# Kernel tuning notes

Measured on AMD Instinct MI355X. Metric: run time of the kernel, lower is better.

## Reference

```python
import jax, jax.numpy as jnp
import numpy as np

C = 64        # in_channels
E = 64        # embed_dim
K_RATIO = 0.5


def _conv(x, w, b, pad, groups):
    # x: [B,C,H,W], w: [O, I/groups, kh, kw] (torch OIHW layout)
    y = jax.lax.conv_general_dilated(
        x, w, window_strides=(1, 1), padding=[(pad, pad), (pad, pad)],
        dimension_numbers=("NCHW", "OIHW", "NCHW"), feature_group_count=groups)
    return y + b[None, :, None, None]


def setup_inputs() -> dict:
    key = jax.random.key(0)
    ks = jax.random.split(key, 16)
    s = 0.05
    return {
        "x": jax.random.normal(ks[0], (8, C, 64, 64), jnp.float32),
        "w1": jax.random.normal(ks[1], (C, C, 1, 1), jnp.float32) * s,
        "b1": jax.random.normal(ks[2], (C,), jnp.float32) * s,
        "w3": jax.random.normal(ks[3], (C, 1, 3, 3), jnp.float32) * s,
        "b3": jax.random.normal(ks[4], (C,), jnp.float32) * s,
        "w5": jax.random.normal(ks[5], (C, 1, 5, 5), jnp.float32) * s,
        "b5": jax.random.normal(ks[6], (C,), jnp.float32) * s,
        "qw": jax.random.normal(ks[7], (E, 3 * C), jnp.float32) * s,
        "qb": jax.random.normal(ks[8], (E,), jnp.float32) * s,
        "kw": jax.random.normal(ks[9], (E, 3 * C), jnp.float32) * s,
        "kb": jax.random.normal(ks[10], (E,), jnp.float32) * s,
        "vw": jax.random.normal(ks[11], (C, 3 * C), jnp.float32) * s,
        "vb": jax.random.normal(ks[12], (C,), jnp.float32) * s,
        "ow": jax.random.normal(ks[13], (C, C), jnp.float32) * s,
        "ob": jax.random.normal(ks[14], (C,), jnp.float32) * s,
    }


def reference(x, w1, b1, w3, b3, w5, b5, qw, qb, kw, kb, vw, vb, ow, ob):
    b, c, h, w = x.shape
    N = h * w
    f1 = _conv(x, w1, b1, pad=0, groups=1)        # 1x1 conv
    f2 = _conv(x, w3, b3, pad=1, groups=c)        # 3x3 depthwise
    f3 = _conv(x, w5, b5, pad=2, groups=c)        # 5x5 depthwise
    f_multi = jnp.concatenate([f1, f2, f3], axis=1)           # [b, 3c, h, w]
    f_flat = f_multi.reshape(b, 3 * c, N).transpose(0, 2, 1)  # [b, N, 3c]

    Q = jnp.einsum("bnd,ed->bne", f_flat, qw) + qb            # [b, N, E]
    K = jnp.einsum("bnd,ed->bne", f_flat, kw) + kb            # [b, N, E]
    V = jnp.einsum("bnd,cd->bnc", f_flat, vw) + vb            # [b, N, c]

    attn = jnp.einsum("bqe,bke->bqk", Q, K) / jnp.sqrt(jnp.float32(E))
    attn = jax.nn.softmax(attn, axis=-1)                      # [b, N, N]

    key_importance = attn.sum(axis=1)                         # [b, N]
    k_val = max(1, min(int(N * K_RATIO), N))
    _, topk_idx = jax.lax.top_k(key_importance, k_val)        # [b, k_val]
    mask = jnp.zeros_like(key_importance).at[
        jnp.arange(b)[:, None], topk_idx].set(1.0)            # [b, N]

    attn_c = attn * mask[:, None, :]
    attn_c = attn_c / (attn_c.sum(axis=-1, keepdims=True) + 1e-8)
    out = jnp.einsum("bqk,bkc->bqc", attn_c, V)               # [b, N, c]
    out = jnp.einsum("bnc,oc->bno", out, ow) + ob
    return out.transpose(0, 2, 1).reshape(b, c, h, w)
```

## Files before the change

### kernel.cpp

```cpp
#include <hip/hip_runtime.h>
#include <hip/hip_bf16.h>

typedef unsigned short ushort;
typedef __bf16 bf16x8 __attribute__((ext_vector_type(8)));
typedef float f32x4 __attribute__((ext_vector_type(4)));

__device__ __forceinline__ ushort f2bu(float f) {
  __hip_bfloat16 h = __float2bfloat16(f);
  return *(ushort*)&h;
}
__device__ __forceinline__ f32x4 mfma16(bf16x8 a, bf16x8 b, f32x4 c) {
  return __builtin_amdgcn_mfma_f32_16x16x32_bf16(a, b, c, 0, 0, 0);
}
__device__ __forceinline__ float fexp2(float x) { return __builtin_amdgcn_exp2f(x); }


__global__ __launch_bounds__(256) void k_conv(
    const float* __restrict__ x, const float* __restrict__ w1, const float* __restrict__ b1,
    const float* __restrict__ w3, const float* __restrict__ b3,
    const float* __restrict__ w5, const float* __restrict__ b5,
    ushort* __restrict__ f) {
  __shared__ float xs[64][64];
  __shared__ float w1s[64 * 65];
  __shared__ float w3s[576];
  __shared__ float w5s[1600];
  __shared__ float bs1[64], bs3[64], bs5[64];
  const int tid = threadIdx.x;
  const int y = blockIdx.x;
  const int b = blockIdx.y;
  for (int i = tid; i < 4096; i += 256) {
    int ch = i >> 6, w = i & 63;
    xs[ch][w] = x[((size_t)(b * 64 + ch) * 64 + y) * 64 + w];
  }
  for (int i = tid; i < 4096; i += 256) w1s[(i >> 6) * 65 + (i & 63)] = w1[i];
  for (int i = tid; i < 576; i += 256) w3s[i] = w3[i];
  for (int i = tid; i < 1600; i += 256) w5s[i] = w5[i];
  if (tid < 64) { bs1[tid] = b1[tid]; bs3[tid] = b3[tid]; bs5[tid] = b5[tid]; }
  __syncthreads();
  const int px = tid & 63;
  const int cg = tid >> 6;
  const int cb = cg * 16;
  ushort* fo = f + ((size_t)b * 4096 + y * 64 + px) * 192;
  float a1[16];
#pragma unroll
  for (int j = 0; j < 16; j++) a1[j] = bs1[cb + j];
  for (int ic = 0; ic < 64; ic++) {
    float xv = xs[ic][px];
#pragma unroll
    for (int j = 0; j < 16; j++) a1[j] += w1s[(cb + j) * 65 + ic] * xv;
  }
#pragma unroll
  for (int j = 0; j < 16; j++) fo[cb + j] = f2bu(a1[j]);
#pragma unroll 4
  for (int j = 0; j < 16; j++) {
    int c = cb + j;
    const float* xc = x + (size_t)(b * 64 + c) * 4096;
    float a3 = bs3[c], a5 = bs5[c];
#pragma unroll
    for (int dy = 0; dy < 5; dy++) {
      int yy = y + dy - 2;
      if (yy < 0 || yy >= 64) continue;
      const float* xr = xc + yy * 64;
#pragma unroll
      for (int dx = 0; dx < 5; dx++) {
        int wx = px + dx - 2;
        float v = (wx >= 0 && wx < 64) ? xr[wx] : 0.f;
        a5 += w5s[c * 25 + dy * 5 + dx] * v;
        if (dy >= 1 && dy <= 3 && dx >= 1 && dx <= 3)
          a3 += w3s[c * 9 + (dy - 1) * 3 + (dx - 1)] * v;
      }
    }
    fo[64 + c] = f2bu(a3);
    fo[128 + c] = f2bu(a5);
  }
}

__global__ __launch_bounds__(256) void k_w2b(
    const float* __restrict__ qw, const float* __restrict__ kw,
    const float* __restrict__ vw, ushort* __restrict__ Wb) {
  int i = blockIdx.x * 256 + threadIdx.x;
  const float* src = (i < 12288) ? qw : (i < 24576) ? kw : vw;
  int off = (i < 12288) ? i : (i < 24576) ? (i - 12288) : (i - 24576);
  Wb[i] = f2bu(src[off]);
}

__global__ __launch_bounds__(256) void k_qkv(
    const ushort* __restrict__ F, const ushort* __restrict__ Wb,
    const float* __restrict__ qb, const float* __restrict__ kb,
    const float* __restrict__ vb,
    ushort* __restrict__ Q, ushort* __restrict__ K, ushort* __restrict__ V) {
  __shared__ __align__(16) ushort fs[64][200];
  const int tid = threadIdx.x;
  const int w = tid >> 6;
  const int lane = tid & 63;
  const int col = lane & 15;
  const int quad = lane >> 4;
  const size_t rowbase = (size_t)blockIdx.x * 64;
  for (int i = tid; i < 1536; i += 256) {
    int r = i / 24, c8 = i % 24;
    *(uint4*)&fs[r][c8 * 8] = *(const uint4*)&F[rowbase * 192 + (size_t)i * 8];
  }
  __syncthreads();
  bf16x8 af[6];
#pragma unroll
  for (int kk = 0; kk < 6; kk++)
    af[kk] = *(const bf16x8*)&fs[w * 16 + col][kk * 32 + quad * 8];
  ushort* const outp[3] = {Q, K, V};
  const float* const bp[3] = {qb, kb, vb};
#pragma unroll
  for (int sel = 0; sel < 3; sel++) {
    const ushort* wsel = Wb + sel * 12288;
    const float sc = (sel == 0) ? 0.125f * 1.44269504088896f : 1.0f;
#pragma unroll
    for (int ntl = 0; ntl < 4; ntl++) {
      const ushort* brow = wsel + (ntl * 16 + col) * 192 + quad * 8;
      f32x4 acc = {0.f, 0.f, 0.f, 0.f};
#pragma unroll
      for (int kk = 0; kk < 6; kk++) {
        bf16x8 bf = *(const bf16x8*)&brow[kk * 32];
        acc = mfma16(af[kk], bf, acc);
      }
      float bv = bp[sel][ntl * 16 + col];
#pragma unroll
      for (int r = 0; r < 4; r++)
        outp[sel][(rowbase + w * 16 + quad * 4 + r) * 64 + ntl * 16 + col] =
            f2bu((acc[r] + bv) * sc);
    }
  }
}

__global__ __launch_bounds__(256) void k_sumexp_l(
    const ushort* __restrict__ Qb, const ushort* __restrict__ Kb,
    float* __restrict__ Lp) {
  __shared__ float red[4][64];
  const int tid = threadIdx.x;
  const int b = blockIdx.x & 7;
  const int rest = blockIdx.x >> 3;
  const int qt = rest & 63;
  const int kh = rest >> 6;
  const int lane = tid & 63;
  const int w = tid >> 6;
  const int col = lane & 15;
  const int quad = lane >> 4;
  const size_t qbase = (size_t)b * 4096 + qt * 64;
  const size_t kbase = (size_t)b * 4096 + kh * 2048;
  bf16x8 af[4][2];
#pragma unroll
  for (int t = 0; t < 4; t++)
#pragma unroll
    for (int h = 0; h < 2; h++)
      af[t][h] = *(const bf16x8*)&Qb[(qbase + t * 16 + col) * 64 + quad * 8 + h * 32];
  const ushort* kp = &Kb[(kbase + w * 16 + col) * 64 + quad * 8];
  float lacc[4][4];
#pragma unroll
  for (int t = 0; t < 4; t++)
#pragma unroll
    for (int r = 0; r < 4; r++) lacc[t][r] = 0.f;
  bf16x8 nb0 = *(const bf16x8*)kp;
  bf16x8 nb1 = *(const bf16x8*)(kp + 32);
#pragma unroll 1
  for (int kt = 0; kt < 32; kt++) {
    bf16x8 b0 = nb0, b1 = nb1;
    if (kt < 31) {
      nb0 = *(const bf16x8*)(kp + (size_t)(kt + 1) * 4096);
      nb1 = *(const bf16x8*)(kp + (size_t)(kt + 1) * 4096 + 32);
    }
#pragma unroll
    for (int t = 0; t < 4; t++) {
      f32x4 acc = {0.f, 0.f, 0.f, 0.f};
      acc = mfma16(af[t][0], b0, acc);
      acc = mfma16(af[t][1], b1, acc);
#pragma unroll
      for (int r = 0; r < 4; r++) lacc[t][r] += fexp2(acc[r]);
    }
  }
#pragma unroll
  for (int t = 0; t < 4; t++)
#pragma unroll
    for (int r = 0; r < 4; r++) {
      float v = lacc[t][r];
      v += __shfl_xor(v, 1); v += __shfl_xor(v, 2);
      v += __shfl_xor(v, 4); v += __shfl_xor(v, 8);
      if (col == 0) red[w][t * 16 + quad * 4 + r] = v;
    }
  __syncthreads();
  if (tid < 64) {
    float l = red[0][tid] + red[1][tid] + red[2][tid] + red[3][tid];
    Lp[((size_t)(b * 64 + qt) * 2 + kh) * 64 + tid] = l;
  }
}

__global__ __launch_bounds__(256) void k_lcomb(
    const float* __restrict__ Lp, float* __restrict__ Lo, float* __restrict__ Linv) {
  int i = blockIdx.x * 256 + threadIdx.x;
  int bqt = i >> 6, q = i & 63;
  float l = Lp[(size_t)bqt * 128 + q] + Lp[(size_t)bqt * 128 + 64 + q];
  Lo[i] = l;
  Linv[i] = 1.f / l;
}

__global__ __launch_bounds__(256) void k_sumexp_ip(
    const ushort* __restrict__ Qb, const ushort* __restrict__ Kb,
    const float* __restrict__ Linv, float* __restrict__ IP) {
  __shared__ float lred[64];
  const int tid = threadIdx.x;
  const int b = blockIdx.x & 7;
  const int rest = blockIdx.x >> 3;
  const int qt = rest & 63;
  const int kh = rest >> 6;
  const int lane = tid & 63;
  const int w = tid >> 6;
  const int col = lane & 15;
  const int quad = lane >> 4;
  const size_t qbase = (size_t)b * 4096 + qt * 64;
  const size_t kbase = (size_t)b * 4096 + kh * 2048;
  if (tid < 64) lred[tid] = Linv[qbase + tid];
  bf16x8 af[4][2];
#pragma unroll
  for (int t = 0; t < 4; t++)
#pragma unroll
    for (int h = 0; h < 2; h++)
      af[t][h] = *(const bf16x8*)&Qb[(qbase + t * 16 + col) * 64 + quad * 8 + h * 32];
  __syncthreads();
  float linv[4][4];
#pragma unroll
  for (int t = 0; t < 4; t++)
#pragma unroll
    for (int r = 0; r < 4; r++) linv[t][r] = lred[t * 16 + quad * 4 + r];
  const ushort* kp = &Kb[(kbase + w * 16 + col) * 64 + quad * 8];
  bf16x8 nb0 = *(const bf16x8*)kp;
  bf16x8 nb1 = *(const bf16x8*)(kp + 32);
#pragma unroll 1
  for (int kt = 0; kt < 32; kt++) {
    bf16x8 b0 = nb0, b1 = nb1;
    if (kt < 31) {
      nb0 = *(const bf16x8*)(kp + (size_t)(kt + 1) * 4096);
      nb1 = *(const bf16x8*)(kp + (size_t)(kt + 1) * 4096 + 32);
    }
    float ip = 0.f;
#pragma unroll
    for (int t = 0; t < 4; t++) {
      f32x4 acc = {0.f, 0.f, 0.f, 0.f};
      acc = mfma16(af[t][0], b0, acc);
      acc = mfma16(af[t][1], b1, acc);
#pragma unroll
      for (int r = 0; r < 4; r++) ip += fexp2(acc[r]) * linv[t][r];
    }
    ip += __shfl_xor(ip, 16);
    ip += __shfl_xor(ip, 32);
    if (quad == 0)
      IP[((size_t)(b * 64 + qt)) * 4096 + (kh * 32 + kt) * 64 + w * 16 + col] = ip;
  }
}

__global__ __launch_bounds__(256) void k_impsum(
    const float* __restrict__ IP, float* __restrict__ imp) {
  const int tid = threadIdx.x;
  const int b = blockIdx.y;
  const int col = blockIdx.x * 256 + tid;
  const float* p = IP + (size_t)b * 64 * 4096 + col;
  float s = 0.f;
#pragma unroll 8
  for (int r = 0; r < 64; r++) s += p[(size_t)r * 4096];
  imp[(size_t)b * 4096 + col] = s;
}

__global__ __launch_bounds__(256) void k_mask2c(
    const float* __restrict__ imp, const ushort* __restrict__ Kb,
    const ushort* __restrict__ Vb, ushort* __restrict__ Kc,
    ushort* __restrict__ Vc) {
  __shared__ __align__(16) float imps[4096];
  __shared__ int part[4][64];
  const int tid = threadIdx.x;
  const int b = blockIdx.y;
  const int base = blockIdx.x * 64;
  for (int i = tid; i < 4096; i += 256) imps[i] = imp[(size_t)b * 4096 + i];
  __syncthreads();
  const int cand = tid & 63;
  const int seg = tid >> 6;
  const int k = base + cand;
  const float v = imps[k];
  int cnt = 0;
  const int j0 = seg * 1024;
  for (int j = j0; j < j0 + 1024; j += 4) {
    float4 a = *(const float4*)&imps[j];
    cnt += (a.x > v) ? 1 : ((a.x == v && (j + 0) < k) ? 1 : 0);
    cnt += (a.y > v) ? 1 : ((a.y == v && (j + 1) < k) ? 1 : 0);
    cnt += (a.z > v) ? 1 : ((a.z == v && (j + 2) < k) ? 1 : 0);
    cnt += (a.w > v) ? 1 : ((a.w == v && (j + 3) < k) ? 1 : 0);
  }
  part[seg][cand] = cnt;
  __syncthreads();
  const int c = part[0][cand] + part[1][cand] + part[2][cand] + part[3][cand];
  if (c < 2048) {
    const ushort* ksrc = &Kb[((size_t)b * 4096 + k) * 64 + seg * 16];
    const ushort* vsrc = &Vb[((size_t)b * 4096 + k) * 64 + seg * 16];
    ushort* kdst = &Kc[((size_t)b * 2048 + c) * 64 + seg * 16];
    ushort* vdst = &Vc[((size_t)b * 2048 + c) * 64 + seg * 16];
    *(uint4*)kdst = *(const uint4*)ksrc;
    *(uint4*)(kdst + 8) = *(const uint4*)(ksrc + 8);
    *(uint4*)vdst = *(const uint4*)vsrc;
    *(uint4*)(vdst + 8) = *(const uint4*)(vsrc + 8);
  }
}

__global__ __launch_bounds__(256) void k_attn_out(
    const ushort* __restrict__ Qb, const ushort* __restrict__ Kc,
    const ushort* __restrict__ Vc, const float* __restrict__ Lo,
    const float* __restrict__ owp, const float* __restrict__ obp,
    float* __restrict__ out) {
  __shared__ __align__(16) ushort Vt[64][72];
  __shared__ __align__(16) ushort Ps[64][72];
  __shared__ __align__(16) ushort ows[64][72];
  __shared__ float dred[4][64];
  __shared__ float lqs[64];
  const int tid = threadIdx.x;
  const int b = blockIdx.x & 7;
  const int qt = blockIdx.x >> 3;
  const int lane = tid & 63;
  const int w = tid >> 6;
  const int col = lane & 15;
  const int quad = lane >> 4;
  const size_t qbase = (size_t)b * 4096 + qt * 64;
  const size_t kbase = (size_t)b * 2048;
  bf16x8 af[4][2];
#pragma unroll
  for (int t = 0; t < 4; t++)
#pragma unroll
    for (int h = 0; h < 2; h++)
      af[t][h] = *(const bf16x8*)&Qb[(qbase + t * 16 + col) * 64 + quad * 8 + h * 32];
  for (int i = tid; i < 4096; i += 256) ows[i >> 6][i & 63] = f2bu(owp[i]);
  if (tid < 64) lqs[tid] = Lo[qbase + tid];
  f32x4 pv[4];
  float dpacc[4][4];
#pragma unroll
  for (int t = 0; t < 4; t++) {
    pv[t] = (f32x4){0.f, 0.f, 0.f, 0.f};
#pragma unroll
    for (int r = 0; r < 4; r++) dpacc[t][r] = 0.f;
  }
  const int vrow = tid & 63;
  const int vch = tid >> 6;
  const ushort* kp = &Kc[(kbase + w * 16 + col) * 64 + quad * 8];
  bf16x8 nb0 = *(const bf16x8*)kp;
  bf16x8 nb1 = *(const bf16x8*)(kp + 32);
  for (int kt = 0; kt < 32; kt++) {
    __syncthreads();
    {
      const ushort* vsrc = &Vc[(kbase + kt * 64 + vrow) * 64 + vch * 16];
      uint4 v0 = *(const uint4*)vsrc;
      uint4 v1 = *(const uint4*)(vsrc + 8);
      ushort tmp[16];
      *(uint4*)&tmp[0] = v0;
      *(uint4*)&tmp[8] = v1;
#pragma unroll
      for (int j = 0; j < 16; j++) Vt[vch * 16 + j][vrow] = tmp[j];
    }
    bf16x8 b0 = nb0, b1 = nb1;
    if (kt < 31) {
      nb0 = *(const bf16x8*)(kp + (size_t)(kt + 1) * 4096);
      nb1 = *(const bf16x8*)(kp + (size_t)(kt + 1) * 4096 + 32);
    }
#pragma unroll
    for (int t = 0; t < 4; t++) {
      f32x4 acc = {0.f, 0.f, 0.f, 0.f};
      acc = mfma16(af[t][0], b0, acc);
      acc = mfma16(af[t][1], b1, acc);
#pragma unroll
      for (int r = 0; r < 4; r++) {
        float p = fexp2(acc[r]);
        dpacc[t][r] += p;
        Ps[t * 16 + quad * 4 + r][w * 16 + col] = f2bu(p);
      }
    }
    __syncthreads();
    bf16x8 v0f = *(const bf16x8*)&Vt[w * 16 + col][quad * 8];
    bf16x8 v1f = *(const bf16x8*)&Vt[w * 16 + col][quad * 8 + 32];
#pragma unroll
    for (int t = 0; t < 4; t++) {
      bf16x8 p0 = *(const bf16x8*)&Ps[t * 16 + col][quad * 8];
      bf16x8 p1 = *(const bf16x8*)&Ps[t * 16 + col][quad * 8 + 32];
      pv[t] = mfma16(p0, v0f, pv[t]);
      pv[t] = mfma16(p1, v1f, pv[t]);
    }
  }
#pragma unroll
  for (int t = 0; t < 4; t++)
#pragma unroll
    for (int r = 0; r < 4; r++) {
      float v = dpacc[t][r];
      v += __shfl_xor(v, 1); v += __shfl_xor(v, 2);
      v += __shfl_xor(v, 4); v += __shfl_xor(v, 8);
      if (col == 0) dred[w][t * 16 + quad * 4 + r] = v;
    }
  __syncthreads();
#pragma unroll
  for (int t = 0; t < 4; t++)
#pragma unroll
    for (int r = 0; r < 4; r++) {
      int q = t * 16 + quad * 4 + r;
      float den = dred[0][q] + dred[1][q] + dred[2][q] + dred[3][q] + 1e-8f * lqs[q];
      Ps[q][w * 16 + col] = f2bu(pv[t][r] / den);
    }
  __syncthreads();
  bf16x8 w0 = *(const bf16x8*)&ows[w * 16 + col][quad * 8];
  bf16x8 w1 = *(const bf16x8*)&ows[w * 16 + col][quad * 8 + 32];
  const float obv = obp[w * 16 + col];
#pragma unroll
  for (int t = 0; t < 4; t++) {
    bf16x8 p0 = *(const bf16x8*)&Ps[t * 16 + col][quad * 8];
    bf16x8 p1 = *(const bf16x8*)&Ps[t * 16 + col][quad * 8 + 32];
    f32x4 oc = {0.f, 0.f, 0.f, 0.f};
    oc = mfma16(p0, w0, oc);
    oc = mfma16(p1, w1, oc);
#pragma unroll
    for (int r = 0; r < 4; r++) {
      int q = t * 16 + quad * 4 + r;
      int co = w * 16 + col;
      out[((size_t)(b * 64 + co)) * 4096 + qt * 64 + q] = oc[r] + obv;
    }
  }
}

extern "C" void kernel_launch(void* const* d_in, const int* in_sizes, int n_in,
                              void* d_out, int out_size, void* d_ws, size_t ws_size,
                              hipStream_t stream) {
  const float* x  = (const float*)d_in[0];
  const float* w1 = (const float*)d_in[1];
  const float* b1 = (const float*)d_in[2];
  const float* w3 = (const float*)d_in[3];
  const float* b3 = (const float*)d_in[4];
  const float* w5 = (const float*)d_in[5];
  const float* b5 = (const float*)d_in[6];
  const float* qw = (const float*)d_in[7];
  const float* qb = (const float*)d_in[8];
  const float* kw = (const float*)d_in[9];
  const float* kb = (const float*)d_in[10];
  const float* vw = (const float*)d_in[11];
  const float* vb = (const float*)d_in[12];
  const float* ow = (const float*)d_in[13];
  const float* ob = (const float*)d_in[14];
  float* out = (float*)d_out;
  float* ws = (float*)d_ws;
  ushort* F    = (ushort*)ws;
  ushort* Qb   = (ushort*)(ws + 3145728);
  ushort* Kb   = (ushort*)(ws + 4194304);
  ushort* Vb   = (ushort*)(ws + 5242880);
  float*  Lo   = ws + 6291456;
  float*  Linv = ws + 6324224;
  float*  Lp   = ws + 6356992;
  float*  IP   = ws + 6422528;
  float*  imp  = ws + 8519680;
  ushort* Kc   = (ushort*)(ws + 8552448);
  ushort* Vc   = (ushort*)(ws + 9076736);
  ushort* Wb   = (ushort*)(ws + 9601024);

  k_w2b<<<144, 256, 0, stream>>>(qw, kw, vw, Wb);
  k_conv<<<dim3(64, 8), 256, 0, stream>>>(x, w1, b1, w3, b3, w5, b5, F);
  k_qkv<<<512, 256, 0, stream>>>(F, Wb, qb, kb, vb, Qb, Kb, Vb);
  k_sumexp_l<<<1024, 256, 0, stream>>>(Qb, Kb, Lp);
  k_lcomb<<<128, 256, 0, stream>>>(Lp, Lo, Linv);
  k_sumexp_ip<<<1024, 256, 0, stream>>>(Qb, Kb, Linv, IP);
  k_impsum<<<dim3(16, 8), 256, 0, stream>>>(IP, imp);
  k_mask2c<<<dim3(64, 8), 256, 0, stream>>>(imp, Kb, Vb, Kc, Vc);
  k_attn_out<<<512, 256, 0, stream>>>(Qb, Kc, Vc, Lo, ow, ob, out);
}
```

Before: 333.8 us.

## Stage padded bf16 input rows in LDS for conv; read transposed 1x1 weights directly

The conv kernel now loads a 5-row halo of the input, converted to bf16, into shared memory with zero padding. The depthwise 3x3/5x5 taps read from LDS instead of strided global memory with bounds checks. The 1x1 conv weights are pre-transposed by the weight-conversion kernel and read with a wave-uniform index from global memory, which drops the weight and bias LDS staging. Rounding the input to bf16 before the convolutions adds precision loss, and each block reloads five rows, so input traffic goes up while the per-tap boundary branches disappear.

```diff
diff --git a/kernel.cpp b/kernel.cpp
--- a/kernel.cpp
+++ b/kernel.cpp
@@ -9,6 +9,10 @@
   __hip_bfloat16 h = __float2bfloat16(f);
   return *(ushort*)&h;
 }
+__device__ __forceinline__ float bu2f(ushort u) {
+  unsigned int v = ((unsigned int)u) << 16;
+  return __uint_as_float(v);
+}
 __device__ __forceinline__ f32x4 mfma16(bf16x8 a, bf16x8 b, f32x4 c) {
   return __builtin_amdgcn_mfma_f32_16x16x32_bf16(a, b, c, 0, 0, 0);
 }
@@ -16,58 +20,61 @@
 
 
 __global__ __launch_bounds__(256) void k_conv(
-    const float* __restrict__ x, const float* __restrict__ w1, const float* __restrict__ b1,
+    const float* __restrict__ x, const float* __restrict__ w1t, const float* __restrict__ b1,
     const float* __restrict__ w3, const float* __restrict__ b3,
     const float* __restrict__ w5, const float* __restrict__ b5,
     ushort* __restrict__ f) {
-  __shared__ float xs[64][64];
-  __shared__ float w1s[64 * 65];
-  __shared__ float w3s[576];
-  __shared__ float w5s[1600];
-  __shared__ float bs1[64], bs3[64], bs5[64];
+  __shared__ ushort Xs[5 * 64 * 74];
   const int tid = threadIdx.x;
   const int y = blockIdx.x;
   const int b = blockIdx.y;
-  for (int i = tid; i < 4096; i += 256) {
-    int ch = i >> 6, w = i & 63;
-    xs[ch][w] = x[((size_t)(b * 64 + ch) * 64 + y) * 64 + w];
-  }
-  for (int i = tid; i < 4096; i += 256) w1s[(i >> 6) * 65 + (i & 63)] = w1[i];
-  for (int i = tid; i < 576; i += 256) w3s[i] = w3[i];
-  for (int i = tid; i < 1600; i += 256) w5s[i] = w5[i];
-  if (tid < 64) { bs1[tid] = b1[tid]; bs3[tid] = b3[tid]; bs5[tid] = b5[tid]; }
+  for (int i = tid; i < 320 * 5; i += 256) {
+    int r = i / 5, pp = i % 5;
+    int col = (pp < 2) ? 2 * pp : 68 + 2 * (pp - 2);
+    *(unsigned int*)&Xs[r * 74 + col] = 0u;
+  }
+#pragma unroll
+  for (int k = 0; k < 20; k++) {
+    int idx = tid + k * 256;
+    int px4 = idx & 15, ch = (idx >> 4) & 63, yy = idx >> 10;
+    int ysrc = y + yy - 2;
+    float4 v = make_float4(0.f, 0.f, 0.f, 0.f);
+    if (ysrc >= 0 && ysrc < 64)
+      v = *(const float4*)&x[(((size_t)(b * 64 + ch) * 64) + ysrc) * 64 + px4 * 4];
+    unsigned int lo = (unsigned int)f2bu(v.x) | ((unsigned int)f2bu(v.y) << 16);
+    unsigned int hi = (unsigned int)f2bu(v.z) | ((unsigned int)f2bu(v.w) << 16);
+    int base = (yy * 64 + ch) * 74 + 4 + px4 * 4;
+    *(unsigned int*)&Xs[base] = lo;
+    *(unsigned int*)&Xs[base + 2] = hi;
+  }
   __syncthreads();
   const int px = tid & 63;
-  const int cg = tid >> 6;
-  const int cb = cg * 16;
+  const int cbu = __builtin_amdgcn_readfirstlane((tid >> 6) * 16);
   ushort* fo = f + ((size_t)b * 4096 + y * 64 + px) * 192;
   float a1[16];
 #pragma unroll
-  for (int j = 0; j < 16; j++) a1[j] = bs1[cb + j];
+  for (int j = 0; j < 16; j++) a1[j] = b1[cbu + j];
   for (int ic = 0; ic < 64; ic++) {
-    float xv = xs[ic][px];
-#pragma unroll
-    for (int j = 0; j < 16; j++) a1[j] += w1s[(cb + j) * 65 + ic] * xv;
-  }
-#pragma unroll
-  for (int j = 0; j < 16; j++) fo[cb + j] = f2bu(a1[j]);
+    float xv = bu2f(Xs[(2 * 64 + ic) * 74 + 4 + px]);
+    const float* wrow = &w1t[ic * 64 + cbu];
+#pragma unroll
+    for (int j = 0; j < 16; j++) a1[j] += wrow[j] * xv;
+  }
+#pragma unroll
+  for (int j = 0; j < 16; j++) fo[cbu + j] = f2bu(a1[j]);
 #pragma unroll 4
   for (int j = 0; j < 16; j++) {
-    int c = cb + j;
-    const float* xc = x + (size_t)(b * 64 + c) * 4096;
-    float a3 = bs3[c], a5 = bs5[c];
+    int c = cbu + j;
+    float a3 = b3[c], a5 = b5[c];
 #pragma unroll
     for (int dy = 0; dy < 5; dy++) {
-      int yy = y + dy - 2;
-      if (yy < 0 || yy >= 64) continue;
-      const float* xr = xc + yy * 64;
+      const ushort* row = &Xs[(dy * 64 + c) * 74 + 2 + px];
 #pragma unroll
       for (int dx = 0; dx < 5; dx++) {
-        int wx = px + dx - 2;
-        float v = (wx >= 0 && wx < 64) ? xr[wx] : 0.f;
-        a5 += w5s[c * 25 + dy * 5 + dx] * v;
+        float v = bu2f(row[dx]);
+        a5 += w5[c * 25 + dy * 5 + dx] * v;
         if (dy >= 1 && dy <= 3 && dx >= 1 && dx <= 3)
-          a3 += w3s[c * 9 + (dy - 1) * 3 + (dx - 1)] * v;
+          a3 += w3[c * 9 + (dy - 1) * 3 + (dx - 1)] * v;
       }
     }
     fo[64 + c] = f2bu(a3);
@@ -77,11 +84,17 @@
 
 __global__ __launch_bounds__(256) void k_w2b(
     const float* __restrict__ qw, const float* __restrict__ kw,
-    const float* __restrict__ vw, ushort* __restrict__ Wb) {
+    const float* __restrict__ vw, const float* __restrict__ w1,
+    ushort* __restrict__ Wb, float* __restrict__ w1t) {
   int i = blockIdx.x * 256 + threadIdx.x;
-  const float* src = (i < 12288) ? qw : (i < 24576) ? kw : vw;
-  int off = (i < 12288) ? i : (i < 24576) ? (i - 12288) : (i - 24576);
-  Wb[i] = f2bu(src[off]);
+  if (i < 36864) {
+    const float* src = (i < 12288) ? qw : (i < 24576) ? kw : vw;
+    int off = (i < 12288) ? i : (i < 24576) ? (i - 12288) : (i - 24576);
+    Wb[i] = f2bu(src[off]);
+  } else {
+    int j = i - 36864;
+    if (j < 4096) w1t[(j & 63) * 64 + (j >> 6)] = w1[j];
+  }
 }
 
 __global__ __launch_bounds__(256) void k_qkv(
@@ -454,9 +467,10 @@
   ushort* Kc   = (ushort*)(ws + 8552448);
   ushort* Vc   = (ushort*)(ws + 9076736);
   ushort* Wb   = (ushort*)(ws + 9601024);
-
-  k_w2b<<<144, 256, 0, stream>>>(qw, kw, vw, Wb);
-  k_conv<<<dim3(64, 8), 256, 0, stream>>>(x, w1, b1, w3, b3, w5, b5, F);
+  float*  w1t  = ws + 9619456;
+
+  k_w2b<<<160, 256, 0, stream>>>(qw, kw, vw, w1, Wb, w1t);
+  k_conv<<<dim3(64, 8), 256, 0, stream>>>(x, w1t, b1, w3, b3, w5, b5, F);
   k_qkv<<<512, 256, 0, stream>>>(F, Wb, qb, kb, vb, Qb, Kb, Vb);
   k_sumexp_l<<<1024, 256, 0, stream>>>(Qb, Kb, Lp);
   k_lcomb<<<128, 256, 0, stream>>>(Lp, Lo, Linv);
```

New measurement: 306.4 us. 8.2% less time.
